# Optimization experiments

Measured on AMD Instinct MI355X. Metric: run time of the kernel, lower is better.

The kernel has to match this reference:

```python
import jax, jax.numpy as jnp
import numpy as np

N, E, D, H = 50000, 400000, 128, 256


def setup_inputs() -> dict:
    key = jax.random.key(0)
    ks = jax.random.split(key, 16)
    s = 0.02
    inp = {
        "x": jax.random.normal(ks[0], (N, D), dtype=jnp.float32),
        "edge_index": jax.random.randint(ks[1], (2, E), 0, N, dtype=jnp.int64),
        "steps": 1,
        # encoder MLP: Linear(D->H), Linear(H->H), relu after each
        "enc_w1": jax.random.normal(ks[2], (H, D), dtype=jnp.float32) * s,
        "enc_b1": jnp.zeros((H,), dtype=jnp.float32),
        "enc_w2": jax.random.normal(ks[3], (H, H), dtype=jnp.float32) * s,
        "enc_b2": jnp.zeros((H,), dtype=jnp.float32),
        # GeneralConv lin_msg (root_weight=False, bias=True)
        "msg_w": jax.random.normal(ks[4], (H, H), dtype=jnp.float32) * s,
        "msg_b": jnp.zeros((H,), dtype=jnp.float32),
        # decoder MLP: Linear(2H->H) relu, Linear(H->D) tanh
        "dec_w1": jax.random.normal(ks[5], (H, 2 * H), dtype=jnp.float32) * s,
        "dec_b1": jnp.zeros((H,), dtype=jnp.float32),
        "dec_w2": jax.random.normal(ks[6], (D, H), dtype=jnp.float32) * s,
        "dec_b2": jnp.zeros((D,), dtype=jnp.float32),
    }
    return inp


def reference(x, edge_index, steps, enc_w1, enc_b1, enc_w2, enc_b2,
              msg_w, msg_b, dec_w1, dec_b1, dec_w2, dec_b2):
    src = edge_index[0]
    dst = edge_index[1]
    n = x.shape[0]
    for _ in range(steps):  # steps is a small static python int
        # encoder MLP (batch_norm=False, dropout=0, relu + relu)
        h = jax.nn.relu(x @ enc_w1.T + enc_b1)
        h = jax.nn.relu(h @ enc_w2.T + enc_b2)
        # GeneralConv: message = lin_msg(x_j); aggr='add'; no root weight
        # lin_msg is edge-independent -> transform on nodes, then gather/scatter
        m = h @ msg_w.T + msg_b                      # [N, H]
        out = jax.ops.segment_sum(m[src], dst, num_segments=n)  # [N, H]
        # decoder on cat(out, h): relu then tanh
        d = jax.nn.relu(jnp.concatenate([out, h], axis=-1) @ dec_w1.T + dec_b1)
        x = jnp.tanh(d @ dec_w2.T + dec_b2)
    return x
```

## Files before the change

### kernel.cpp

```cpp
#include <hip/hip_runtime.h>
#include <cmath>


typedef __attribute__((ext_vector_type(8))) short  short8;
typedef __attribute__((ext_vector_type(4))) float  f32x4;
typedef __attribute__((ext_vector_type(4))) unsigned short us4;

typedef unsigned short u16;
typedef unsigned int   u32;

static __device__ __forceinline__ u16 f2bf(float f) {
    u32 u = __float_as_uint(f);
    u = (u + 0x7FFFu + ((u >> 16) & 1u)) >> 16;
    return (u16)u;
}
static __device__ __forceinline__ float bf2f(u16 h) {
    return __uint_as_float(((u32)h) << 16);
}

static __device__ __forceinline__ void g2l16(const void* g, void* l) {
    __builtin_amdgcn_global_load_lds(
        (const __attribute__((address_space(1))) u32*)g,
        (__attribute__((address_space(3))) u32*)l, 16, 0, 0);
}

__global__ __launch_bounds__(512, 2) void enc_fused(
    const float* __restrict__ x, const u16* __restrict__ w1,
    const float* __restrict__ b1, const u16* __restrict__ w2,
    const float* __restrict__ b2, const u16* __restrict__ wm,
    const float* __restrict__ bm, u16* __restrict__ hout,
    u16* __restrict__ mout, const int N, const int ntiles)
{
    __shared__ u16 hL[8][4][512];

    const int t    = threadIdx.x;
    const int wave = t >> 6;
    const int lane = t & 63;
    const int n    = lane & 15;
    const int q    = lane >> 4;
    const int wc   = wave * 32;

    short8 b1f[4][2];
#pragma unroll
    for (int c = 0; c < 4; c++)
#pragma unroll
        for (int j = 0; j < 2; j++)
            b1f[c][j] = *reinterpret_cast<const short8*>(
                w1 + (size_t)(wc + j * 16 + n) * 128 + c * 32 + q * 8);
    short8 bW[8][2];
#pragma unroll
    for (int c = 0; c < 8; c++)
#pragma unroll
        for (int j = 0; j < 2; j++)
            bW[c][j] = *reinterpret_cast<const short8*>(
                w2 + (size_t)(wc + j * 16 + n) * 256 + c * 32 + q * 8);
    const float bv1_0 = b1[wc + n], bv1_1 = b1[wc + 16 + n];
    const float bv2_0 = b2[wc + n], bv2_1 = b2[wc + 16 + n];
    const float bvm_0 = bm[wc + n], bvm_1 = bm[wc + 16 + n];

    const int xcol   = (t & 31) * 4;
    const int xrow0  = t >> 5;
    const int xchunk = xcol >> 5;
    const int xidx   = (((xcol >> 3) & 3) * 16 + xrow0) * 8 + (xcol & 7);

    float4 xr[4];
    int tile = blockIdx.x;
#pragma unroll
    for (int kk = 0; kk < 4; kk++) {
        const int gr = min(tile * 64 + xrow0 + kk * 16, N - 1);
        xr[kk] = *reinterpret_cast<const float4*>(x + (size_t)gr * 128 + xcol);
    }

    for (;;) {
        const int r0 = tile * 64;

#pragma unroll
        for (int kk = 0; kk < 4; kk++) {
            us4 o = { f2bf(xr[kk].x), f2bf(xr[kk].y),
                      f2bf(xr[kk].z), f2bf(xr[kk].w) };
            *reinterpret_cast<us4*>(&hL[4 + xchunk][kk][xidx]) = o;
        }
        __syncthreads();

        const int ntile = tile + 256;
        if (ntile < ntiles) {
#pragma unroll
            for (int kk = 0; kk < 4; kk++) {
                const int gr = min(ntile * 64 + xrow0 + kk * 16, N - 1);
                xr[kk] = *reinterpret_cast<const float4*>(
                    x + (size_t)gr * 128 + xcol);
            }
        }

        f32x4 acc[4][2];
#pragma unroll
        for (int i = 0; i < 4; i++)
#pragma unroll
            for (int j = 0; j < 2; j++) acc[i][j] = (f32x4)0.0f;

#pragma unroll
        for (int c = 0; c < 4; c++) {
            short8 af[4];
#pragma unroll
            for (int i = 0; i < 4; i++)
                af[i] = *reinterpret_cast<const short8*>(
                    &hL[4 + c][i][lane * 8]);
#pragma unroll
            for (int i = 0; i < 4; i++)
#pragma unroll
                for (int j = 0; j < 2; j++)
                    acc[i][j] = __builtin_amdgcn_mfma_f32_16x16x32_bf16(
                        af[i], b1f[c][j], acc[i][j], 0, 0, 0);
        }

        short8 bp[4][2];
#pragma unroll
        for (int c = 0; c < 4; c++)
#pragma unroll
            for (int j = 0; j < 2; j++)
                bp[c][j] = *reinterpret_cast<const short8*>(
                    wm + (size_t)(wc + j * 16 + n) * 256 + c * 32 + q * 8);

        __syncthreads();

        {
            const int np = q * 4;
#pragma unroll
            for (int i = 0; i < 4; i++)
#pragma unroll
                for (int reg = 0; reg < 4; reg++) {
#pragma unroll
                    for (int j = 0; j < 2; j++) {
                        const float v = fmaxf(
                            acc[i][j][reg] + (j ? bv1_1 : bv1_0), 0.0f);
                        const int q2 = j * 2 + (n >> 3);
                        hL[wave][i][(q2 * 16 + np + reg) * 8 + (n & 7)] =
                            f2bf(v);
                    }
                }
        }
        __syncthreads();

#pragma unroll
        for (int i = 0; i < 4; i++)
#pragma unroll
            for (int j = 0; j < 2; j++) acc[i][j] = (f32x4)0.0f;
#pragma unroll
        for (int c = 0; c < 8; c++) {
            short8 af[4];
#pragma unroll
            for (int i = 0; i < 4; i++)
                af[i] = *reinterpret_cast<const short8*>(&hL[c][i][lane * 8]);
#pragma unroll
            for (int i = 0; i < 4; i++)
#pragma unroll
                for (int j = 0; j < 2; j++)
                    acc[i][j] = __builtin_amdgcn_mfma_f32_16x16x32_bf16(
                        af[i], bW[c][j], acc[i][j], 0, 0, 0);
        }

        {
            const int np = q * 4;
#pragma unroll
            for (int i = 0; i < 4; i++)
#pragma unroll
                for (int reg = 0; reg < 4; reg++) {
                    const int row = r0 + i * 16 + q * 4 + reg;
                    if (row < N) {
                        hout[(size_t)row * 256 + wc + n] =
                            f2bf(fmaxf(acc[i][0][reg] + bv2_0, 0.0f));
                        hout[(size_t)row * 256 + wc + 16 + n] =
                            f2bf(fmaxf(acc[i][1][reg] + bv2_1, 0.0f));
                    }
                }
            __syncthreads();
#pragma unroll
            for (int i = 0; i < 4; i++)
#pragma unroll
                for (int reg = 0; reg < 4; reg++) {
#pragma unroll
                    for (int j = 0; j < 2; j++) {
                        const float v = fmaxf(
                            acc[i][j][reg] + (j ? bv2_1 : bv2_0), 0.0f);
                        const int q2 = j * 2 + (n >> 3);
                        hL[wave][i][(q2 * 16 + np + reg) * 8 + (n & 7)] =
                            f2bf(v);
                    }
                }
        }
        __syncthreads();

#pragma unroll
        for (int i = 0; i < 4; i++)
#pragma unroll
            for (int j = 0; j < 2; j++) acc[i][j] = (f32x4)0.0f;
#pragma unroll
        for (int c = 0; c < 8; c++) {
            short8 af[4];
#pragma unroll
            for (int i = 0; i < 4; i++)
                af[i] = *reinterpret_cast<const short8*>(&hL[c][i][lane * 8]);
#pragma unroll
            for (int i = 0; i < 4; i++)
#pragma unroll
                for (int j = 0; j < 2; j++)
                    acc[i][j] = __builtin_amdgcn_mfma_f32_16x16x32_bf16(
                        af[i], bp[c & 3][j], acc[i][j], 0, 0, 0);
            if (c < 4) {
#pragma unroll
                for (int j = 0; j < 2; j++)
                    bp[c][j] = *reinterpret_cast<const short8*>(
                        wm + (size_t)(wc + j * 16 + n) * 256 +
                        (c + 4) * 32 + q * 8);
            }
        }
        {
#pragma unroll
            for (int i = 0; i < 4; i++)
#pragma unroll
                for (int reg = 0; reg < 4; reg++) {
                    const int row = r0 + i * 16 + q * 4 + reg;
                    if (row < N) {
                        mout[(size_t)row * 256 + wc + n] =
                            f2bf(acc[i][0][reg] + bvm_0);
                        mout[(size_t)row * 256 + wc + 16 + n] =
                            f2bf(acc[i][1][reg] + bvm_1);
                    }
                }
        }

        tile = ntile;
        if (tile >= ntiles) break;
        __syncthreads();
    }
}

__global__ __launch_bounds__(512, 4) void dec_fused(
    const u16* __restrict__ aggr, const u16* __restrict__ h,
    const u16* __restrict__ wd1, const float* __restrict__ bd1,
    const u16* __restrict__ wd2, const float* __restrict__ bd2,
    float* __restrict__ out, const int N)
{
    __shared__ u16 dL[8][4][512];

    const int t    = threadIdx.x;
    const int r0   = blockIdx.x * 64;
    const int wave = t >> 6;
    const int lane = t & 63;
    const int n    = lane & 15;
    const int q    = lane >> 4;
    const int wc   = wave * 32;

    const int w4   = wave & 3;
    const int sub  = wave >> 2;
    const int srow = min(r0 + w4 * 16 + (lane & 15), N - 1);
    const int kq8  = (lane >> 4) * 8;
    const u16* aptr = aggr + (size_t)srow * 256 + kq8;
    const u16* hptr = h    + (size_t)srow * 256 + kq8;

#define DEC_STAGE(p, buf)                                                   \
    {                                                                       \
        const int c_  = 2 * (p) + sub;                                      \
        const int kc_ = c_ * 32;                                            \
        const u16* sp_ = (kc_ < 256) ? (aptr + kc_) : (hptr + (kc_ - 256)); \
        g2l16(sp_, &dL[(buf) * 2 + sub][w4][0]);                            \
    }

    f32x4 acc[4][2];
#pragma unroll
    for (int i = 0; i < 4; i++)
#pragma unroll
        for (int j = 0; j < 2; j++) acc[i][j] = (f32x4)0.0f;

    DEC_STAGE(0, 0);
    short8 bp[4][2];
#pragma unroll
    for (int c = 0; c < 4; c++)
#pragma unroll
        for (int j = 0; j < 2; j++)
            bp[c][j] = *reinterpret_cast<const short8*>(
                wd1 + (size_t)(wc + j * 16 + n) * 512 + c * 32 + q * 8);
    __syncthreads();

#pragma unroll
    for (int p = 0; p < 8; p++) {
        if (p < 7) DEC_STAGE(p + 1, (p + 1) & 1);
#pragma unroll
        for (int s = 0; s < 2; s++) {
            const int c = 2 * p + s;
            short8 af[4];
#pragma unroll
            for (int i = 0; i < 4; i++)
                af[i] = *reinterpret_cast<const short8*>(
                    &dL[(p & 1) * 2 + s][i][lane * 8]);
#pragma unroll
            for (int i = 0; i < 4; i++)
#pragma unroll
                for (int j = 0; j < 2; j++)
                    acc[i][j] = __builtin_amdgcn_mfma_f32_16x16x32_bf16(
                        af[i], bp[c & 3][j], acc[i][j], 0, 0, 0);
            if (c + 4 < 16) {
#pragma unroll
                for (int j = 0; j < 2; j++)
                    bp[c & 3][j] = *reinterpret_cast<const short8*>(
                        wd1 + (size_t)(wc + j * 16 + n) * 512 +
                        (c + 4) * 32 + q * 8);
            }
        }
        __syncthreads();
    }
#undef DEC_STAGE

    {
        const float bv0 = bd1[wc + n];
        const float bv1 = bd1[wc + 16 + n];
        const int np = q * 4;
#pragma unroll
        for (int i = 0; i < 4; i++)
#pragma unroll
            for (int reg = 0; reg < 4; reg++) {
#pragma unroll
                for (int j = 0; j < 2; j++) {
                    const float v = fmaxf(acc[i][j][reg] + (j ? bv1 : bv0), 0.0f);
                    const int q2 = j * 2 + (n >> 3);
                    dL[wave][i][(q2 * 16 + np + reg) * 8 + (n & 7)] = f2bf(v);
                }
            }
    }

    const int wc2 = wave * 16;
    short8 b2p[4];
#pragma unroll
    for (int c = 0; c < 4; c++)
        b2p[c] = *reinterpret_cast<const short8*>(
            wd2 + (size_t)(wc2 + n) * 256 + c * 32 + q * 8);
    __syncthreads();

    f32x4 acc2[4];
#pragma unroll
    for (int i = 0; i < 4; i++) acc2[i] = (f32x4)0.0f;
#pragma unroll
    for (int c = 0; c < 8; c++) {
        short8 af[4], bf;
#pragma unroll
        for (int i = 0; i < 4; i++)
            af[i] = *reinterpret_cast<const short8*>(&dL[c][i][lane * 8]);
        bf = b2p[c & 3];
#pragma unroll
        for (int i = 0; i < 4; i++)
            acc2[i] = __builtin_amdgcn_mfma_f32_16x16x32_bf16(
                af[i], bf, acc2[i], 0, 0, 0);
        if (c < 4)
            b2p[c] = *reinterpret_cast<const short8*>(
                wd2 + (size_t)(wc2 + n) * 256 + (c + 4) * 32 + q * 8);
    }
    {
        const float bv = bd2[wc2 + n];
#pragma unroll
        for (int i = 0; i < 4; i++)
#pragma unroll
            for (int reg = 0; reg < 4; reg++) {
                const int row = r0 + i * 16 + q * 4 + reg;
                if (row < N)
                    out[(size_t)row * 128 + wc2 + n] = tanhf(acc2[i][reg] + bv);
            }
    }
}

__global__ __launch_bounds__(256) void cvt6_kernel(
    const float* s0, const float* s1, const float* s2, const float* s3,
    const float* s4,
    u16* d0, u16* d1, u16* d2, u16* d3, u16* d4,
    int* __restrict__ zp,
    int n0, int n1, int n2, int n3, int n4, int nz)
{
    const int i = blockIdx.x * 256 + threadIdx.x;
    if (blockIdx.y == 5) {
        if (i < nz) zp[i] = 0;
        return;
    }
    const float* s; u16* d; int nq;
    switch (blockIdx.y) {
        case 0: s = s0; d = d0; nq = n0; break;
        case 1: s = s1; d = d1; nq = n1; break;
        case 2: s = s2; d = d2; nq = n2; break;
        case 3: s = s3; d = d3; nq = n3; break;
        default: s = s4; d = d4; nq = n4; break;
    }
    if (i < nq) {
        const float4 v = reinterpret_cast<const float4*>(s)[i];
        us4 o = { f2bf(v.x), f2bf(v.y), f2bf(v.z), f2bf(v.w) };
        reinterpret_cast<us4*>(d)[i] = o;
    }
}

__global__ __launch_bounds__(256) void fill_kernel(
    const int* __restrict__ ei, int* __restrict__ cursor,
    int* __restrict__ bucket, const int E, const int Nn)
{
    const int e = blockIdx.x * 256 + threadIdx.x;
    if (e < E) {
        const int src = ei[e];
        const int dst = ei[(size_t)E + e];
        if ((unsigned)dst < (unsigned)Nn) {
            const int pos = atomicAdd(&cursor[dst], 1);
            if (pos < 64) bucket[(size_t)dst * 64 + pos] = src;
        }
    }
}

__global__ __launch_bounds__(256) void gather_sum_kernel(
    const u16* __restrict__ m, const int* __restrict__ bucket,
    const int* __restrict__ cursor, u16* __restrict__ outa, const int Nn)
{
    const int wave = (int)((blockIdx.x * 256u + threadIdx.x) >> 6);
    const int lane = threadIdx.x & 63;
    if (wave >= Nn) return;
    const int cnt = min(cursor[wave], 64);
    const int* bl = bucket + (size_t)wave * 64;
    float a0 = 0.f, a1 = 0.f, a2 = 0.f, a3 = 0.f;
    for (int base = 0; base < cnt; base += 8) {
        int sidx[8];
#pragma unroll
        for (int u = 0; u < 8; u++)
            sidx[u] = (base + u < cnt) ? bl[base + u] : -1;
        us4 v[8];
#pragma unroll
        for (int u = 0; u < 8; u++) {
            const int s = ((unsigned)sidx[u] < (unsigned)Nn) ? sidx[u] : 0;
            v[u] = *reinterpret_cast<const us4*>(&m[(size_t)s * 256 + lane * 4]);
        }
#pragma unroll
        for (int u = 0; u < 8; u++) {
            if ((unsigned)sidx[u] < (unsigned)Nn) {
                a0 += bf2f(v[u].x); a1 += bf2f(v[u].y);
                a2 += bf2f(v[u].z); a3 += bf2f(v[u].w);
            }
        }
    }
    us4 o = { f2bf(a0), f2bf(a1), f2bf(a2), f2bf(a3) };
    *reinterpret_cast<us4*>(&outa[(size_t)wave * 256 + lane * 4]) = o;
}

extern "C" void kernel_launch(void* const* d_in, const int* in_sizes, int n_in,
                              void* d_out, int out_size, void* d_ws, size_t ws_size,
                              hipStream_t stream)
{
    const float* x      = (const float*)d_in[0];
    const int*   ei     = (const int*)d_in[1];
    const float* enc_w1 = (const float*)d_in[3];
    const float* enc_b1 = (const float*)d_in[4];
    const float* enc_w2 = (const float*)d_in[5];
    const float* enc_b2 = (const float*)d_in[6];
    const float* msg_w  = (const float*)d_in[7];
    const float* msg_b  = (const float*)d_in[8];
    const float* dec_w1 = (const float*)d_in[9];
    const float* dec_b1 = (const float*)d_in[10];
    const float* dec_w2 = (const float*)d_in[11];
    const float* dec_b2 = (const float*)d_in[12];

    const int N = 50000, D = 128, H = 256;
    const int E = in_sizes[1] / 2;

    u16* h    = (u16*)d_ws;
    u16* m    = h    + (size_t)N * H;
    u16* aggr = m    + (size_t)N * H;
    u16* w1   = aggr + (size_t)N * H;
    u16* w2   = w1 + 256 * 128;
    u16* wm   = w2 + 256 * 256;
    u16* wd1  = wm + 256 * 256;
    u16* wd2  = wd1 + 256 * 512;
    int* cursor = (int*)(wd2 + 128 * 256);
    int* bucket = cursor + N;

    const dim3 blk(256);
    const dim3 blk512(512);
    const int ntiles = (N + 63) / 64;
    const int nb64 = ntiles;
    const int cvtx = (N + 255) / 256;

    cvt6_kernel<<<dim3(cvtx, 6), blk, 0, stream>>>(
        enc_w1, enc_w2, msg_w, dec_w1, dec_w2,
        w1, w2, wm, wd1, wd2, cursor,
        256 * 128 / 4, 256 * 256 / 4, 256 * 256 / 4,
        256 * 512 / 4, 128 * 256 / 4, N);

    fill_kernel<<<dim3((E + 255) / 256), blk, 0, stream>>>(
        ei, cursor, bucket, E, N);

    enc_fused<<<dim3(256), blk512, 0, stream>>>(
        x, w1, enc_b1, w2, enc_b2, wm, msg_b, h, m, N, ntiles);

    gather_sum_kernel<<<dim3((N * 64 + 255) / 256), blk, 0, stream>>>(
        m, bucket, cursor, aggr, N);

    dec_fused<<<dim3(nb64), blk512, 0, stream>>>(
        aggr, h, wd1, dec_b1, wd2, dec_b2, (float*)d_out, N);
}
```

Measured before the change: 248.8 us.

## Fold message linear into decoder weights and gather h instead of m

The edge-independent message linear is moved past the segment sum: the kernel gathers h directly and precomputes Wc = dec_w1[:, :H] @ msg_w plus a degree-scaled bias term, which the decoder's first layer applies. This removes the third GEMM and the N×H m buffer write from the encoder. It also shrinks bucket indices to 16 bits to cut traffic. The 16-bit indices only work while N < 65536, and the folded weight is rounded to bf16, which adds some precision risk.

```diff
diff --git a/kernel.cpp b/kernel.cpp
--- a/kernel.cpp
+++ b/kernel.cpp
@@ -27,9 +27,8 @@
 __global__ __launch_bounds__(512, 2) void enc_fused(
     const float* __restrict__ x, const u16* __restrict__ w1,
     const float* __restrict__ b1, const u16* __restrict__ w2,
-    const float* __restrict__ b2, const u16* __restrict__ wm,
-    const float* __restrict__ bm, u16* __restrict__ hout,
-    u16* __restrict__ mout, const int N, const int ntiles)
+    const float* __restrict__ b2, u16* __restrict__ hout,
+    const int N, const int ntiles)
 {
     __shared__ u16 hL[8][4][512];
 
@@ -56,7 +55,6 @@
                 w2 + (size_t)(wc + j * 16 + n) * 256 + c * 32 + q * 8);
     const float bv1_0 = b1[wc + n], bv1_1 = b1[wc + 16 + n];
     const float bv2_0 = b2[wc + n], bv2_1 = b2[wc + 16 + n];
-    const float bvm_0 = bm[wc + n], bvm_1 = bm[wc + 16 + n];
 
     const int xcol   = (t & 31) * 4;
     const int xrow0  = t >> 5;
@@ -112,15 +110,6 @@
                     acc[i][j] = __builtin_amdgcn_mfma_f32_16x16x32_bf16(
                         af[i], b1f[c][j], acc[i][j], 0, 0, 0);
         }
-
-        short8 bp[4][2];
-#pragma unroll
-        for (int c = 0; c < 4; c++)
-#pragma unroll
-            for (int j = 0; j < 2; j++)
-                bp[c][j] = *reinterpret_cast<const short8*>(
-                    wm + (size_t)(wc + j * 16 + n) * 256 + c * 32 + q * 8);
-
         __syncthreads();
 
         {
@@ -160,7 +149,6 @@
         }
 
         {
-            const int np = q * 4;
 #pragma unroll
             for (int i = 0; i < 4; i++)
 #pragma unroll
@@ -173,60 +161,6 @@
                             f2bf(fmaxf(acc[i][1][reg] + bv2_1, 0.0f));
                     }
                 }
-            __syncthreads();
-#pragma unroll
-            for (int i = 0; i < 4; i++)
-#pragma unroll
-                for (int reg = 0; reg < 4; reg++) {
-#pragma unroll
-                    for (int j = 0; j < 2; j++) {
-                        const float v = fmaxf(
-                            acc[i][j][reg] + (j ? bv2_1 : bv2_0), 0.0f);
-                        const int q2 = j * 2 + (n >> 3);
-                        hL[wave][i][(q2 * 16 + np + reg) * 8 + (n & 7)] =
-                            f2bf(v);
-                    }
-                }
-        }
-        __syncthreads();
-
-#pragma unroll
-        for (int i = 0; i < 4; i++)
-#pragma unroll
-            for (int j = 0; j < 2; j++) acc[i][j] = (f32x4)0.0f;
-#pragma unroll
-        for (int c = 0; c < 8; c++) {
-            short8 af[4];
-#pragma unroll
-            for (int i = 0; i < 4; i++)
-                af[i] = *reinterpret_cast<const short8*>(&hL[c][i][lane * 8]);
-#pragma unroll
-            for (int i = 0; i < 4; i++)
-#pragma unroll
-                for (int j = 0; j < 2; j++)
-                    acc[i][j] = __builtin_amdgcn_mfma_f32_16x16x32_bf16(
-                        af[i], bp[c & 3][j], acc[i][j], 0, 0, 0);
-            if (c < 4) {
-#pragma unroll
-                for (int j = 0; j < 2; j++)
-                    bp[c][j] = *reinterpret_cast<const short8*>(
-                        wm + (size_t)(wc + j * 16 + n) * 256 +
-                        (c + 4) * 32 + q * 8);
-            }
-        }
-        {
-#pragma unroll
-            for (int i = 0; i < 4; i++)
-#pragma unroll
-                for (int reg = 0; reg < 4; reg++) {
-                    const int row = r0 + i * 16 + q * 4 + reg;
-                    if (row < N) {
-                        mout[(size_t)row * 256 + wc + n] =
-                            f2bf(acc[i][0][reg] + bvm_0);
-                        mout[(size_t)row * 256 + wc + 16 + n] =
-                            f2bf(acc[i][1][reg] + bvm_1);
-                    }
-                }
         }
 
         tile = ntile;
@@ -236,12 +170,15 @@
 }
 
 __global__ __launch_bounds__(512, 4) void dec_fused(
-    const u16* __restrict__ aggr, const u16* __restrict__ h,
-    const u16* __restrict__ wd1, const float* __restrict__ bd1,
+    const u16* __restrict__ g, const u16* __restrict__ h,
+    const u16* __restrict__ wcb, const u16* __restrict__ wd1,
+    const float* __restrict__ bd1, const float* __restrict__ bc,
+    const int* __restrict__ cursor,
     const u16* __restrict__ wd2, const float* __restrict__ bd2,
     float* __restrict__ out, const int N)
 {
     __shared__ u16 dL[8][4][512];
+    __shared__ float degL[64];
 
     const int t    = threadIdx.x;
     const int r0   = blockIdx.x * 64;
@@ -255,8 +192,8 @@
     const int sub  = wave >> 2;
     const int srow = min(r0 + w4 * 16 + (lane & 15), N - 1);
     const int kq8  = (lane >> 4) * 8;
-    const u16* aptr = aggr + (size_t)srow * 256 + kq8;
-    const u16* hptr = h    + (size_t)srow * 256 + kq8;
+    const u16* aptr = g + (size_t)srow * 256 + kq8;
+    const u16* hptr = h + (size_t)srow * 256 + kq8;
 
 #define DEC_STAGE(p, buf)                                                   \
     {                                                                       \
@@ -266,6 +203,19 @@
         g2l16(sp_, &dL[(buf) * 2 + sub][w4][0]);                            \
     }
 
+#define BFRAG(cc, j)                                                        \
+    ((cc) < 8                                                               \
+     ? *reinterpret_cast<const short8*>(                                    \
+           wcb + (size_t)(wc + (j) * 16 + n) * 256 + (cc) * 32 + q * 8)     \
+     : *reinterpret_cast<const short8*>(                                    \
+           wd1 + (size_t)(wc + (j) * 16 + n) * 512 + 256 +                  \
+           ((cc) - 8) * 32 + q * 8))
+
+    if (t < 64) {
+        const int cc = cursor[min(r0 + t, N - 1)];
+        degL[t] = (float)(cc > 64 ? 64 : cc);
+    }
+
     f32x4 acc[4][2];
 #pragma unroll
     for (int i = 0; i < 4; i++)
@@ -277,9 +227,7 @@
 #pragma unroll
     for (int c = 0; c < 4; c++)
 #pragma unroll
-        for (int j = 0; j < 2; j++)
-            bp[c][j] = *reinterpret_cast<const short8*>(
-                wd1 + (size_t)(wc + j * 16 + n) * 512 + c * 32 + q * 8);
+        for (int j = 0; j < 2; j++) bp[c][j] = BFRAG(c, j);
     __syncthreads();
 
 #pragma unroll
@@ -302,26 +250,30 @@
             if (c + 4 < 16) {
 #pragma unroll
                 for (int j = 0; j < 2; j++)
-                    bp[c & 3][j] = *reinterpret_cast<const short8*>(
-                        wd1 + (size_t)(wc + j * 16 + n) * 512 +
-                        (c + 4) * 32 + q * 8);
+                    bp[c & 3][j] = BFRAG(c + 4, j);
             }
         }
         __syncthreads();
     }
 #undef DEC_STAGE
+#undef BFRAG
 
     {
         const float bv0 = bd1[wc + n];
         const float bv1 = bd1[wc + 16 + n];
+        const float bc0 = bc[wc + n];
+        const float bc1 = bc[wc + 16 + n];
         const int np = q * 4;
 #pragma unroll
         for (int i = 0; i < 4; i++)
 #pragma unroll
             for (int reg = 0; reg < 4; reg++) {
+                const float dv = degL[i * 16 + q * 4 + reg];
 #pragma unroll
                 for (int j = 0; j < 2; j++) {
-                    const float v = fmaxf(acc[i][j][reg] + (j ? bv1 : bv0), 0.0f);
+                    const float v = fmaxf(
+                        acc[i][j][reg] + (j ? bv1 : bv0) +
+                        dv * (j ? bc1 : bc0), 0.0f);
                     const int q2 = j * 2 + (n >> 3);
                     dL[wave][i][(q2 * 16 + np + reg) * 8 + (n & 7)] = f2bf(v);
                 }
@@ -367,15 +319,36 @@
     }
 }
 
-__global__ __launch_bounds__(256) void cvt6_kernel(
+__global__ __launch_bounds__(256) void wc_kernel(
+    const float* __restrict__ wd1f, const float* __restrict__ wmf,
+    const float* __restrict__ bmf, u16* __restrict__ wcb,
+    float* __restrict__ bc)
+{
+    __shared__ float red[256];
+    const int o = blockIdx.x;
+    const int j = threadIdx.x;
+    const float* wrow = wd1f + (size_t)o * 512;
+    float acc = 0.0f;
+    for (int k = 0; k < 256; k++)
+        acc = fmaf(wrow[k], wmf[(size_t)k * 256 + j], acc);
+    wcb[(size_t)o * 256 + j] = f2bf(acc);
+    red[j] = wrow[j] * bmf[j];
+    __syncthreads();
+    for (int st = 128; st > 0; st >>= 1) {
+        if (j < st) red[j] += red[j + st];
+        __syncthreads();
+    }
+    if (j == 0) bc[o] = red[0];
+}
+
+__global__ __launch_bounds__(256) void cvt5_kernel(
     const float* s0, const float* s1, const float* s2, const float* s3,
-    const float* s4,
-    u16* d0, u16* d1, u16* d2, u16* d3, u16* d4,
+    u16* d0, u16* d1, u16* d2, u16* d3,
     int* __restrict__ zp,
-    int n0, int n1, int n2, int n3, int n4, int nz)
+    int n0, int n1, int n2, int n3, int nz)
 {
     const int i = blockIdx.x * 256 + threadIdx.x;
-    if (blockIdx.y == 5) {
+    if (blockIdx.y == 4) {
         if (i < nz) zp[i] = 0;
         return;
     }
@@ -384,8 +357,7 @@
         case 0: s = s0; d = d0; nq = n0; break;
         case 1: s = s1; d = d1; nq = n1; break;
         case 2: s = s2; d = d2; nq = n2; break;
-        case 3: s = s3; d = d3; nq = n3; break;
-        default: s = s4; d = d4; nq = n4; break;
+        default: s = s3; d = d3; nq = n3; break;
     }
     if (i < nq) {
         const float4 v = reinterpret_cast<const float4*>(s)[i];
@@ -396,7 +368,7 @@
 
 __global__ __launch_bounds__(256) void fill_kernel(
     const int* __restrict__ ei, int* __restrict__ cursor,
-    int* __restrict__ bucket, const int E, const int Nn)
+    u16* __restrict__ bucket, const int E, const int Nn)
 {
     const int e = blockIdx.x * 256 + threadIdx.x;
     if (e < E) {
@@ -404,42 +376,42 @@
         const int dst = ei[(size_t)E + e];
         if ((unsigned)dst < (unsigned)Nn) {
             const int pos = atomicAdd(&cursor[dst], 1);
-            if (pos < 64) bucket[(size_t)dst * 64 + pos] = src;
+            if (pos < 64) bucket[(size_t)dst * 64 + pos] = (u16)src;
         }
     }
 }
 
 __global__ __launch_bounds__(256) void gather_sum_kernel(
-    const u16* __restrict__ m, const int* __restrict__ bucket,
-    const int* __restrict__ cursor, u16* __restrict__ outa, const int Nn)
+    const u16* __restrict__ h, const u16* __restrict__ bucket,
+    const int* __restrict__ cursor, u16* __restrict__ outg, const int Nn)
 {
     const int wave = (int)((blockIdx.x * 256u + threadIdx.x) >> 6);
     const int lane = threadIdx.x & 63;
     if (wave >= Nn) return;
     const int cnt = min(cursor[wave], 64);
-    const int* bl = bucket + (size_t)wave * 64;
+    const u16* bl = bucket + (size_t)wave * 64;
     float a0 = 0.f, a1 = 0.f, a2 = 0.f, a3 = 0.f;
     for (int base = 0; base < cnt; base += 8) {
         int sidx[8];
 #pragma unroll
         for (int u = 0; u < 8; u++)
-            sidx[u] = (base + u < cnt) ? bl[base + u] : -1;
+            sidx[u] = (base + u < cnt) ? (int)bl[base + u] : 0x10000;
         us4 v[8];
 #pragma unroll
         for (int u = 0; u < 8; u++) {
-            const int s = ((unsigned)sidx[u] < (unsigned)Nn) ? sidx[u] : 0;
-            v[u] = *reinterpret_cast<const us4*>(&m[(size_t)s * 256 + lane * 4]);
+            const int s = (sidx[u] < Nn) ? sidx[u] : 0;
+            v[u] = *reinterpret_cast<const us4*>(&h[(size_t)s * 256 + lane * 4]);
         }
 #pragma unroll
         for (int u = 0; u < 8; u++) {
-            if ((unsigned)sidx[u] < (unsigned)Nn) {
+            if (sidx[u] < Nn) {
                 a0 += bf2f(v[u].x); a1 += bf2f(v[u].y);
                 a2 += bf2f(v[u].z); a3 += bf2f(v[u].w);
             }
         }
     }
     us4 o = { f2bf(a0), f2bf(a1), f2bf(a2), f2bf(a3) };
-    *reinterpret_cast<us4*>(&outa[(size_t)wave * 256 + lane * 4]) = o;
+    *reinterpret_cast<us4*>(&outg[(size_t)wave * 256 + lane * 4]) = o;
 }
 
 extern "C" void kernel_launch(void* const* d_in, const int* in_sizes, int n_in,
@@ -463,37 +435,37 @@
     const int E = in_sizes[1] / 2;
 
     u16* h    = (u16*)d_ws;
-    u16* m    = h    + (size_t)N * H;
-    u16* aggr = m    + (size_t)N * H;
-    u16* w1   = aggr + (size_t)N * H;
+    u16* g    = h   + (size_t)N * H;
+    u16* w1   = g   + (size_t)N * H;
     u16* w2   = w1 + 256 * 128;
-    u16* wm   = w2 + 256 * 256;
-    u16* wd1  = wm + 256 * 256;
+    u16* wd1  = w2 + 256 * 256;
     u16* wd2  = wd1 + 256 * 512;
-    int* cursor = (int*)(wd2 + 128 * 256);
-    int* bucket = cursor + N;
+    u16* wcb  = wd2 + 128 * 256;
+    float* bc = (float*)(wcb + 256 * 256);
+    int* cursor = (int*)(bc + 256);
+    u16* bucket = (u16*)(cursor + N);
 
     const dim3 blk(256);
     const dim3 blk512(512);
     const int ntiles = (N + 63) / 64;
-    const int nb64 = ntiles;
     const int cvtx = (N + 255) / 256;
 
-    cvt6_kernel<<<dim3(cvtx, 6), blk, 0, stream>>>(
-        enc_w1, enc_w2, msg_w, dec_w1, dec_w2,
-        w1, w2, wm, wd1, wd2, cursor,
-        256 * 128 / 4, 256 * 256 / 4, 256 * 256 / 4,
-        256 * 512 / 4, 128 * 256 / 4, N);
+    cvt5_kernel<<<dim3(cvtx, 5), blk, 0, stream>>>(
+        enc_w1, enc_w2, dec_w1, dec_w2,
+        w1, w2, wd1, wd2, cursor,
+        256 * 128 / 4, 256 * 256 / 4, 256 * 512 / 4, 128 * 256 / 4, N);
+
+    wc_kernel<<<dim3(256), blk, 0, stream>>>(dec_w1, msg_w, msg_b, wcb, bc);
 
     fill_kernel<<<dim3((E + 255) / 256), blk, 0, stream>>>(
         ei, cursor, bucket, E, N);
 
     enc_fused<<<dim3(256), blk512, 0, stream>>>(
-        x, w1, enc_b1, w2, enc_b2, wm, msg_b, h, m, N, ntiles);
+        x, w1, enc_b1, w2, enc_b2, h, N, ntiles);
 
     gather_sum_kernel<<<dim3((N * 64 + 255) / 256), blk, 0, stream>>>(
-        m, bucket, cursor, aggr, N);
-
-    dec_fused<<<dim3(nb64), blk512, 0, stream>>>(
-        aggr, h, wd1, dec_b1, wd2, dec_b2, (float*)d_out, N);
-}
+        h, bucket, cursor, g, N);
+
+    dec_fused<<<dim3(ntiles), blk512, 0, stream>>>(
+        g, h, wcb, wd1, dec_b1, bc, cursor, wd2, dec_b2, (float*)d_out, N);
+}
```

After: 235.2 us. -5.5%, faster.
